# Kernel optimization log

Hardware: AMD Instinct MI355X
Metric: run time of the kernel (lower is better)

## Reference

```python
import jax, jax.numpy as jnp
import numpy as np

EMBED = 1024
HEADS = 16
HEAD_DIM = EMBED // HEADS
WINDOW = 1024
HALF = WINDOW // 2  # effective causal lookback per token is HALF (window positions > i are masked)
SCALE = HEAD_DIM ** -0.5
B, T = 2, 4096


def setup_inputs() -> dict:
    key = jax.random.key(0)
    ks = jax.random.split(key, 11)
    f = jnp.float32
    return {
        'query': jax.random.normal(ks[0], (B, T, EMBED), f),
        'key':   jax.random.normal(ks[1], (B, T, EMBED), f),
        'value': jax.random.normal(ks[2], (B, T, EMBED), f),
        'wq': jax.random.normal(ks[3], (EMBED, EMBED), f) * 0.02,
        'bq': jax.random.normal(ks[4], (EMBED,), f) * 0.02,
        'wk': jax.random.normal(ks[5], (EMBED, EMBED), f) * 0.02,
        'bk': jax.random.normal(ks[6], (EMBED,), f) * 0.02,
        'wv': jax.random.normal(ks[7], (EMBED, EMBED), f) * 0.02,
        'bv': jax.random.normal(ks[8], (EMBED,), f) * 0.02,
        'wo': jax.random.normal(ks[9], (EMBED, EMBED), f) * 0.02,
        'bo': jax.random.normal(ks[10], (EMBED,), f) * 0.02,
    }


def _sliding_window_attn(q, k, v):
    # q,k,v: [B,H,T,D]; each query i attends to keys j with i-HALF <= j <= i.
    # Blocked formulation with block size Bk=HALF: block b attends to blocks b-1 and b.
    Bq, H, Tq, D = q.shape
    Bk = HALF
    nb = Tq // Bk  # T chosen to be a multiple of HALF
    qb = q.reshape(Bq, H, nb, Bk, D)

    def ctx(x):
        xb = x.reshape(Bq, H, nb, Bk, D)
        prev = jnp.concatenate([jnp.zeros_like(xb[:, :, :1]), xb[:, :, :-1]], axis=2)
        return jnp.concatenate([prev, xb], axis=3)  # [B,H,nb,2Bk,D]

    kc, vc = ctx(k), ctx(v)
    scores = jnp.einsum('bhnrd,bhncd->bhnrc', qb, kc)  # [B,H,nb,Bk,2Bk]
    r = jnp.arange(Bk)[:, None]          # query pos within block
    c = jnp.arange(2 * Bk)[None, :]      # key pos within [prev|cur] context
    # global diff = (Bk + r) - c; valid iff 0 <= diff <= HALF  <=>  r <= c <= r + Bk
    band = (c >= r) & (c <= r + Bk)      # [Bk, 2Bk]
    b_idx = jnp.arange(nb)[:, None, None]
    valid = band[None] & ((b_idx > 0) | (c[None] >= Bk))  # first block has no prev keys
    neg_inf = jnp.finfo(jnp.float32).min
    scores = jnp.where(valid[None, None], scores.astype(jnp.float32), neg_inf)
    attn = jax.nn.softmax(scores, axis=-1).astype(q.dtype)
    out = jnp.einsum('bhnrc,bhncd->bhnrd', attn, vc)
    return out.reshape(Bq, H, Tq, D)


def reference(query, key, value, wq, bq, wk, bk, wv, bv, wo, bo):
    Bq, Tq, C = query.shape
    split = lambda x: x.reshape(Bq, Tq, HEADS, HEAD_DIM).transpose(0, 2, 1, 3)
    q = split(jnp.einsum('btc,oc->bto', query, wq) + bq) * SCALE
    k = split(jnp.einsum('btc,oc->bto', key, wk) + bk)
    v = split(jnp.einsum('btc,oc->bto', value, wv) + bv)
    o = _sliding_window_attn(q, k, v)                       # [B,H,T,D]
    o = o.transpose(0, 2, 1, 3).reshape(Bq, Tq, C)
    return jnp.einsum('btc,oc->bto', o, wo) + bo
```

## Files before the change

### kernel.cpp

```cpp
#include <hip/hip_runtime.h>
#include <hip/hip_bf16.h>

typedef __attribute__((ext_vector_type(8))) short short8;
typedef __attribute__((ext_vector_type(4))) float f32x4;

__device__ __forceinline__ unsigned short f2bf(float f) {
  union { float f; unsigned int u; } x; x.f = f;
  unsigned int r = x.u + 0x7fffu + ((x.u >> 16) & 1u);
  return (unsigned short)(r >> 16);
}

__device__ __forceinline__ float fexp2(float x) {
#if __has_builtin(__builtin_amdgcn_exp2f)
  return __builtin_amdgcn_exp2f(x);
#else
  float r;
  asm("v_exp_f32 %0, %1" : "=v"(r) : "v"(x));
  return r;
#endif
}

#define MFMA16(a, b, c) __builtin_amdgcn_mfma_f32_16x16x32_bf16((a), (b), (c), 0, 0, 0)

__device__ __forceinline__ void gload_lds16(const void* g, void* l) {
  __builtin_amdgcn_global_load_lds((const __attribute__((address_space(1))) void*)g,
                                   (__attribute__((address_space(3))) void*)l, 16, 0, 0);
}

#define WAIT_VM(n) asm volatile("s_waitcnt vmcnt(" #n ")" ::: "memory")
#define RAW_BAR() asm volatile("s_barrier" ::: "memory")

__device__ __forceinline__ void p32swap(unsigned int& a, unsigned int& b) {
  asm volatile("v_permlane32_swap_b32 %0, %1" : "+v"(a), "+v"(b));
}
__device__ __forceinline__ void p16swap(unsigned int& a, unsigned int& b) {
  asm volatile("v_permlane16_swap_b32 %0, %1" : "+v"(a), "+v"(b));
}

#define QSCALE 0.1803368801111244f

__global__ __launch_bounds__(256) void cvt_all(
    const float* __restrict__ q, const float* __restrict__ k,
    const float* __restrict__ v, const float* __restrict__ w0,
    const float* __restrict__ w1, const float* __restrict__ w2,
    const float* __restrict__ w3, unsigned short* __restrict__ Tb,
    unsigned short* __restrict__ Kc, unsigned short* __restrict__ Vc,
    unsigned short* __restrict__ Wb) {
  const int lin = blockIdx.x;
  const float* src;
  unsigned short* dst;
  int i0;
  if (lin < 4096)        { src = q;  dst = Tb;                i0 = lin; }
  else if (lin < 8192)   { src = k;  dst = Kc;                i0 = lin - 4096; }
  else if (lin < 12288)  { src = v;  dst = Vc;                i0 = lin - 8192; }
  else if (lin < 12800)  { src = w0; dst = Wb;                i0 = lin - 12288; }
  else if (lin < 13312)  { src = w1; dst = Wb + (1u << 20);   i0 = lin - 12800; }
  else if (lin < 13824)  { src = w2; dst = Wb + (2u << 20);   i0 = lin - 13312; }
  else                   { src = w3; dst = Wb + (3u << 20);   i0 = lin - 13824; }
  const size_t i = (size_t)i0 * 256 + threadIdx.x;
  const float4* p = (const float4*)src + 2 * i;
  float4 a = p[0], b = p[1];
  ushort4 lo, hi;
  lo.x = f2bf(a.x); lo.y = f2bf(a.y); lo.z = f2bf(a.z); lo.w = f2bf(a.w);
  hi.x = f2bf(b.x); hi.y = f2bf(b.y); hi.z = f2bf(b.z); hi.w = f2bf(b.w);
  ((ushort4*)dst)[2 * i] = lo;
  ((ushort4*)dst)[2 * i + 1] = hi;
}

template <bool SWAP>
__device__ __forceinline__ void gemm_core(const unsigned short* __restrict__ A,
                                          const unsigned short* __restrict__ W,
                                          unsigned short (*As)[128 * 64],
                                          unsigned short (*Bs)[128 * 64],
                                          int bm, int bn, f32x4 (&acc)[2][4]) {
  const int tid = threadIdx.x, lane = tid & 63, wid = tid >> 6;
  const int g = lane >> 4, li = lane & 15;
  const int wr = wid >> 1, wc = wid & 1;
  const int trow = tid >> 3;
  const int js = (tid & 7) ^ (trow & 7);

  auto stage = [&](int kt, int pb) {
    const int k0 = kt << 6;
    #pragma unroll
    for (int r = 0; r < 2; ++r) {
      const int row = r * 64 + trow;
      gload_lds16(A + (size_t)(bm * 128 + row) * 1024 + k0 + js * 8,
                  &As[pb][(r * 64 + wid * 8) * 64]);
      gload_lds16(W + (size_t)(bn * 128 + row) * 1024 + k0 + js * 8,
                  &Bs[pb][(r * 64 + wid * 8) * 64]);
    }
  };

  stage(0, 0);
  int p = 0;
  for (int kt = 0; kt < 16; ++kt) {
    if (kt < 15) {
      stage(kt + 1, p ^ 1);
      WAIT_VM(4);
    } else {
      WAIT_VM(0);
    }
    RAW_BAR();
    #pragma unroll
    for (int kst = 0; kst < 2; ++kst) {
      short8 a[2], b[4];
      #pragma unroll
      for (int mi = 0; mi < 2; ++mi) {
        const int row = wr * 32 + mi * 16 + li;
        a[mi] = *(const short8*)((const char*)&As[p][0] + row * 128 +
                                 (((kst * 4 + g) ^ (li & 7)) << 4));
      }
      #pragma unroll
      for (int ni = 0; ni < 4; ++ni) {
        const int row = wc * 64 + ni * 16 + li;
        b[ni] = *(const short8*)((const char*)&Bs[p][0] + row * 128 +
                                 (((kst * 4 + g) ^ (li & 7)) << 4));
      }
      __builtin_amdgcn_s_setprio(1);
      #pragma unroll
      for (int mi = 0; mi < 2; ++mi)
        #pragma unroll
        for (int ni = 0; ni < 4; ++ni) {
          if constexpr (SWAP)
            acc[mi][ni] = MFMA16(b[ni], a[mi], acc[mi][ni]);
          else
            acc[mi][ni] = MFMA16(a[mi], b[ni], acc[mi][ni]);
        }
      __builtin_amdgcn_s_setprio(0);
    }
    RAW_BAR();
    p ^= 1;
  }
}

__global__ __launch_bounds__(512) void qkv_gemm(
    const unsigned short* __restrict__ Aq, const unsigned short* __restrict__ Ak,
    const unsigned short* __restrict__ Av, const unsigned short* __restrict__ Wb,
    const float* __restrict__ bq, const float* __restrict__ bk,
    const float* __restrict__ bv, unsigned short* __restrict__ Qw,
    unsigned short* __restrict__ Kw, unsigned short* __restrict__ Vw) {
  __shared__ unsigned short As[2][128 * 64];
  __shared__ unsigned short Bs[2][128 * 64];
  const int z = blockIdx.z;
  const int bm = blockIdx.x, bn = blockIdx.y;
  const unsigned short* A = (z == 0) ? Aq : (z == 1) ? Ak : Av;
  const unsigned short* W = Wb + ((size_t)z << 20);
  const float* bias = (z == 0) ? bq : (z == 1) ? bk : bv;
  unsigned short* outp = (z == 0) ? Qw : (z == 1) ? Kw : Vw;

  const int tid = threadIdx.x, lane = tid & 63, wid = tid >> 6;
  const int g = lane >> 4, li = lane & 15;
  const int wr = wid >> 1, wc = wid & 1;

  f32x4 acc[2][4] = {};
  if (z == 2)
    gemm_core<true>(A, W, As, Bs, bm, bn, acc);
  else
    gemm_core<false>(A, W, As, Bs, bm, bn, acc);

  if (z == 2) {
    #pragma unroll
    for (int mi = 0; mi < 2; ++mi) {
      const int mm = bm * 128 + wr * 32 + mi * 16 + li;
      const int b_ = mm >> 12, t_ = mm & 4095;
      #pragma unroll
      for (int ni = 0; ni < 4; ++ni)
        #pragma unroll
        for (int r = 0; r < 4; ++r) {
          const int nn = bn * 128 + wc * 64 + ni * 16 + g * 4 + r;
          const int h_ = nn >> 6, d_ = nn & 63;
          float v = acc[mi][ni][r] + bias[nn];
          outp[(((size_t)(b_ * 16 + h_) * 64 + d_) << 12) + t_] = f2bf(v);
        }
    }
  } else {
    const float scale = (z == 0) ? QSCALE : 1.0f;
    #pragma unroll
    for (int mi = 0; mi < 2; ++mi)
      #pragma unroll
      for (int ni = 0; ni < 4; ++ni) {
        const int nn = bn * 128 + wc * 64 + ni * 16 + li;
        const float bv_ = bias[nn];
        #pragma unroll
        for (int r = 0; r < 4; ++r) {
          const int mm = bm * 128 + wr * 32 + mi * 16 + g * 4 + r;
          const float v = (acc[mi][ni][r] + bv_) * scale;
          const int b_ = mm >> 12, t_ = mm & 4095, h_ = nn >> 6, d_ = nn & 63;
          outp[(((size_t)(b_ * 16 + h_) * 4096 + t_) << 6) + d_] = f2bf(v);
        }
      }
  }
}

__global__ __launch_bounds__(512) void out_gemm(const unsigned short* __restrict__ A,
                                                const unsigned short* __restrict__ W,
                                                const float* __restrict__ bias,
                                                float* __restrict__ outp) {
  __shared__ unsigned short As[2][128 * 64];
  __shared__ unsigned short Bs[2][128 * 64];
  const int bm = blockIdx.x, bn = blockIdx.y;
  const int tid = threadIdx.x, lane = tid & 63, wid = tid >> 6;
  const int g = lane >> 4, li = lane & 15;
  const int wr = wid >> 1, wc = wid & 1;
  f32x4 acc[2][4] = {};
  gemm_core<false>(A, W, As, Bs, bm, bn, acc);
  #pragma unroll
  for (int mi = 0; mi < 2; ++mi)
    #pragma unroll
    for (int ni = 0; ni < 4; ++ni) {
      const int nn = bn * 128 + wc * 64 + ni * 16 + li;
      const float bv_ = bias[nn];
      #pragma unroll
      for (int r = 0; r < 4; ++r) {
        const int mm = bm * 128 + wr * 32 + mi * 16 + g * 4 + r;
        outp[(size_t)mm * 1024 + nn] = acc[mi][ni][r] + bv_;
      }
    }
}

__global__ __launch_bounds__(256) void swa_attn(const unsigned short* __restrict__ Q,
                                                const unsigned short* __restrict__ K,
                                                const unsigned short* __restrict__ V,
                                                unsigned short* __restrict__ O) {
  __shared__ unsigned short Kb[2][4096];
  __shared__ unsigned short Vb[2][4096];
  const int tid = threadIdx.x, lane = tid & 63, w = tid >> 6;
  const int g = lane >> 4, li = lane & 15;
  const int lin = blockIdx.x;
  const int xcd = lin & 7;
  const int rest = lin >> 3;
  const int qoff = rest & 7;
  const int grp = rest >> 3;
  const int G = xcd * 16 + grp;
  const int hb = G & 31;
  const int qb = (G >> 5) * 8 + qoff;
  const int qs = qb << 7;
  const int h = hb & 15, b = hb >> 4;
  const int bh = b * 16 + h;
  const unsigned short* Qh = Q + ((size_t)bh << 18);
  const unsigned short* Kh = K + ((size_t)bh << 18);
  const unsigned short* Vh = V + ((size_t)bh << 18);

  short8 qa[2][2];
  #pragma unroll
  for (int qt = 0; qt < 2; ++qt)
    #pragma unroll
    for (int kst = 0; kst < 2; ++kst)
      qa[qt][kst] =
          *(const short8*)&Qh[((size_t)(qs + w * 32 + qt * 16 + li) << 6) + kst * 32 + g * 8];

  const short8 vone = {0x3F80, 0x3F80, 0x3F80, 0x3F80, 0x3F80, 0x3F80, 0x3F80, 0x3F80};
  f32x4 o[2][4] = {};
  f32x4 lac[2] = {};
  const int c0 = (qs >= 512) ? 0 : ((512 - qs) >> 6);

  const int srow_hi = lane >> 3;
  const int sj = lane & 7;

  auto stage = [&](int c, int pb) {
    const int ks = qs - 512 + (c << 6);
    #pragma unroll
    for (int i = 0; i < 2; ++i) {
      const int seg = w + i * 4;
      const int row = seg * 8 + srow_hi;
      const int jsw = sj ^ (row & 7);
      gload_lds16(Kh + (((size_t)(ks + row)) << 6) + jsw * 8, &Kb[pb][seg * 512]);
      gload_lds16(Vh + (((size_t)row) << 12) + ks + jsw * 8, &Vb[pb][seg * 512]);
    }
  };

  int p = 0;
  stage(c0, 0);

  for (int c = c0; c <= 9; ++c) {
    if (c < 9) {
      stage(c + 1, p ^ 1);
      WAIT_VM(4);
    } else {
      WAIT_VM(0);
    }
    RAW_BAR();
    const int cb = c << 6;
    const bool anyq = (cb + 63 >= w * 32) && (cb <= w * 32 + 543);
    if (anyq) {
      short8 kf[4][2], vf[4][2];
      #pragma unroll
      for (int nt = 0; nt < 4; ++nt) {
        const int row = nt * 16 + li, rx = li & 7;
        #pragma unroll
        for (int kst = 0; kst < 2; ++kst) {
          const int byt = row * 128 + (((kst * 4 + g) ^ rx) << 4);
          kf[nt][kst] = *(const short8*)((const char*)&Kb[p][0] + byt);
          vf[nt][kst] = *(const short8*)((const char*)&Vb[p][0] + byt);
        }
      }
      #pragma unroll
      for (int qt = 0; qt < 2; ++qt) {
        const int base = w * 32 + qt * 16;
        if (cb + 63 < base || cb > base + 527) continue;
        f32x4 s[4];
        __builtin_amdgcn_s_setprio(1);
        #pragma unroll
        for (int nt = 0; nt < 4; ++nt) {
          f32x4 z = {};
          s[nt] = MFMA16(kf[nt][0], qa[qt][0], z);
          s[nt] = MFMA16(kf[nt][1], qa[qt][1], s[nt]);
        }
        __builtin_amdgcn_s_setprio(0);
        if (cb < base + 16 || cb + 63 > base + 512) {
          #pragma unroll
          for (int nt = 0; nt < 4; ++nt)
            #pragma unroll
            for (int r = 0; r < 4; ++r) {
              const int t1 = cb + nt * 16 + g * 4 + r - base;
              if (t1 < li || t1 > 512 + li) s[nt][r] = -3e38f;
            }
        }
        unsigned int pw[4][2];
        #pragma unroll
        for (int nt = 0; nt < 4; ++nt) {
          float2 ab; ab.x = fexp2(s[nt][0]); ab.y = fexp2(s[nt][1]);
          float2 cd; cd.x = fexp2(s[nt][2]); cd.y = fexp2(s[nt][3]);
          union { __hip_bfloat162 h2; unsigned int u; } u0, u1;
          u0.h2 = __float22bfloat162_rn(ab);
          u1.h2 = __float22bfloat162_rn(cd);
          pw[nt][0] = u0.u;
          pw[nt][1] = u1.u;
        }
        short8 pbf[2];
        #pragma unroll
        for (int kst = 0; kst < 2; ++kst) {
          unsigned int A0 = pw[2 * kst][0], B0 = pw[2 * kst + 1][0];
          unsigned int A1 = pw[2 * kst][1], B1 = pw[2 * kst + 1][1];
          p32swap(A0, B0);
          p32swap(A1, B1);
          p16swap(A0, B0);
          p16swap(A1, B1);
          union { unsigned int u[4]; short8 s8; } pb_;
          pb_.u[0] = A0;
          pb_.u[1] = A1;
          pb_.u[2] = B0;
          pb_.u[3] = B1;
          pbf[kst] = pb_.s8;
        }
        __builtin_amdgcn_s_setprio(1);
        lac[qt] = MFMA16(vone, pbf[0], lac[qt]);
        lac[qt] = MFMA16(vone, pbf[1], lac[qt]);
        #pragma unroll
        for (int dt = 0; dt < 4; ++dt) {
          o[qt][dt] = MFMA16(vf[dt][0], pbf[0], o[qt][dt]);
          o[qt][dt] = MFMA16(vf[dt][1], pbf[1], o[qt][dt]);
        }
        __builtin_amdgcn_s_setprio(0);
      }
    }
    RAW_BAR();
    p ^= 1;
  }

  #pragma unroll
  for (int qt = 0; qt < 2; ++qt) {
    const float inv = 1.0f / lac[qt][0];
    const int t_ = qs + w * 32 + qt * 16 + li;
    #pragma unroll
    for (int dt = 0; dt < 4; ++dt) {
      ushort4 u;
      u.x = f2bf(o[qt][dt][0] * inv); u.y = f2bf(o[qt][dt][1] * inv);
      u.z = f2bf(o[qt][dt][2] * inv); u.w = f2bf(o[qt][dt][3] * inv);
      *(ushort4*)&O[((size_t)(b * 4096 + t_) << 10) + h * 64 + dt * 16 + g * 4] = u;
    }
  }
}

extern "C" void kernel_launch(void* const* d_in, const int* in_sizes, int n_in,
                              void* d_out, int out_size, void* d_ws, size_t ws_size,
                              hipStream_t stream) {
  const float* q_in = (const float*)d_in[0];
  const float* k_in = (const float*)d_in[1];
  const float* v_in = (const float*)d_in[2];
  const float* wq = (const float*)d_in[3];
  const float* bq = (const float*)d_in[4];
  const float* wk = (const float*)d_in[5];
  const float* bk = (const float*)d_in[6];
  const float* wv = (const float*)d_in[7];
  const float* bv = (const float*)d_in[8];
  const float* wo = (const float*)d_in[9];
  const float* bo = (const float*)d_in[10];

  unsigned short* Qw = (unsigned short*)d_ws;
  unsigned short* Kw = Qw + (size_t)8388608;
  unsigned short* Vw = Kw + (size_t)8388608;
  unsigned short* Tb = Vw + (size_t)8388608;
  unsigned short* Wb = Tb + (size_t)8388608;
  unsigned short* Kc = (unsigned short*)d_out;
  unsigned short* Vc = Kc + (size_t)8388608;

  dim3 bb(256), bg(512);
  cvt_all<<<14336, bb, 0, stream>>>(q_in, k_in, v_in, wq, wk, wv, wo,
                                    Tb, Kc, Vc, Wb);
  qkv_gemm<<<dim3(64, 8, 3), bg, 0, stream>>>(Tb, Kc, Vc, Wb, bq, bk, bv,
                                              Qw, Kw, Vw);
  swa_attn<<<1024, bb, 0, stream>>>(Qw, Kw, Vw, Tb);
  out_gemm<<<dim3(64, 8), bg, 0, stream>>>(Tb, Wb + (3u << 20), bo,
                                           (float*)d_out);
}
```

Before: 152.0 us.

## Double attention query tile to 256 rows per block with 8 waves

The sliding-window attention kernel now runs 512-thread blocks, each covering 256 queries instead of 128. K/V are staged 128 keys at a time (two 64-key sub-chunks per double-buffered stage) into doubled LDS buffers. Each staged K/V window is therefore shared by twice as many queries, which cuts redundant K/V global loads and the number of barrier rounds. In exchange the grid halves to 512 blocks, LDS per block doubles, and waves at the edges of the block sit idle for more of the key chunks.

```diff
diff --git a/kernel.cpp b/kernel.cpp
--- a/kernel.cpp
+++ b/kernel.cpp
@@ -218,12 +218,12 @@
     }
 }
 
-__global__ __launch_bounds__(256) void swa_attn(const unsigned short* __restrict__ Q,
+__global__ __launch_bounds__(512) void swa_attn(const unsigned short* __restrict__ Q,
                                                 const unsigned short* __restrict__ K,
                                                 const unsigned short* __restrict__ V,
                                                 unsigned short* __restrict__ O) {
-  __shared__ unsigned short Kb[2][4096];
-  __shared__ unsigned short Vb[2][4096];
+  __shared__ unsigned short Kb[2][8192];
+  __shared__ unsigned short Vb[2][8192];
   const int tid = threadIdx.x, lane = tid & 63, w = tid >> 6;
   const int g = lane >> 4, li = lane & 15;
   const int lin = blockIdx.x;
@@ -231,10 +231,10 @@
   const int rest = lin >> 3;
   const int qoff = rest & 7;
   const int grp = rest >> 3;
-  const int G = xcd * 16 + grp;
+  const int G = xcd * 8 + grp;
   const int hb = G & 31;
   const int qb = (G >> 5) * 8 + qoff;
-  const int qs = qb << 7;
+  const int qs = qb << 8;
   const int h = hb & 15, b = hb >> 4;
   const int bh = b * 16 + h;
   const unsigned short* Qh = Q + ((size_t)bh << 18);
@@ -253,109 +253,115 @@
   f32x4 o[2][4] = {};
   f32x4 lac[2] = {};
   const int c0 = (qs >= 512) ? 0 : ((512 - qs) >> 6);
+  const int p0 = c0 >> 1;
 
   const int srow_hi = lane >> 3;
   const int sj = lane & 7;
 
-  auto stage = [&](int c, int pb) {
-    const int ks = qs - 512 + (c << 6);
-    #pragma unroll
-    for (int i = 0; i < 2; ++i) {
-      const int seg = w + i * 4;
-      const int row = seg * 8 + srow_hi;
+  auto stage = [&](int pi, int pb) {
+    const int ks0 = qs - 512 + (pi << 7);
+    #pragma unroll
+    for (int s = 0; s < 2; ++s) {
+      const int row = w * 8 + srow_hi;
       const int jsw = sj ^ (row & 7);
-      gload_lds16(Kh + (((size_t)(ks + row)) << 6) + jsw * 8, &Kb[pb][seg * 512]);
-      gload_lds16(Vh + (((size_t)row) << 12) + ks + jsw * 8, &Vb[pb][seg * 512]);
+      gload_lds16(Kh + (((size_t)(ks0 + s * 64 + row)) << 6) + jsw * 8,
+                  &Kb[pb][s * 4096 + w * 512]);
+      gload_lds16(Vh + (((size_t)row) << 12) + ks0 + s * 64 + jsw * 8,
+                  &Vb[pb][s * 4096 + w * 512]);
     }
   };
 
-  int p = 0;
-  stage(c0, 0);
-
-  for (int c = c0; c <= 9; ++c) {
-    if (c < 9) {
-      stage(c + 1, p ^ 1);
+  int pb = 0;
+  stage(p0, 0);
+
+  for (int pi = p0; pi <= 5; ++pi) {
+    if (pi < 5) {
+      stage(pi + 1, pb ^ 1);
       WAIT_VM(4);
     } else {
       WAIT_VM(0);
     }
     RAW_BAR();
-    const int cb = c << 6;
-    const bool anyq = (cb + 63 >= w * 32) && (cb <= w * 32 + 543);
-    if (anyq) {
-      short8 kf[4][2], vf[4][2];
-      #pragma unroll
-      for (int nt = 0; nt < 4; ++nt) {
-        const int row = nt * 16 + li, rx = li & 7;
+    #pragma unroll
+    for (int s = 0; s < 2; ++s) {
+      const int c = 2 * pi + s;
+      const int cb = c << 6;
+      const bool anyq = (cb + 63 >= w * 32) && (cb <= w * 32 + 543);
+      if (anyq) {
+        short8 kf[4][2], vf[4][2];
         #pragma unroll
-        for (int kst = 0; kst < 2; ++kst) {
-          const int byt = row * 128 + (((kst * 4 + g) ^ rx) << 4);
-          kf[nt][kst] = *(const short8*)((const char*)&Kb[p][0] + byt);
-          vf[nt][kst] = *(const short8*)((const char*)&Vb[p][0] + byt);
+        for (int nt = 0; nt < 4; ++nt) {
+          const int row = nt * 16 + li, rx = li & 7;
+          #pragma unroll
+          for (int kst = 0; kst < 2; ++kst) {
+            const int byt = s * 8192 + row * 128 + (((kst * 4 + g) ^ rx) << 4);
+            kf[nt][kst] = *(const short8*)((const char*)&Kb[pb][0] + byt);
+            vf[nt][kst] = *(const short8*)((const char*)&Vb[pb][0] + byt);
+          }
+        }
+        #pragma unroll
+        for (int qt = 0; qt < 2; ++qt) {
+          const int base = w * 32 + qt * 16;
+          if (cb + 63 < base || cb > base + 527) continue;
+          f32x4 sv[4];
+          __builtin_amdgcn_s_setprio(1);
+          #pragma unroll
+          for (int nt = 0; nt < 4; ++nt) {
+            f32x4 z = {};
+            sv[nt] = MFMA16(kf[nt][0], qa[qt][0], z);
+            sv[nt] = MFMA16(kf[nt][1], qa[qt][1], sv[nt]);
+          }
+          __builtin_amdgcn_s_setprio(0);
+          if (cb < base + 16 || cb + 63 > base + 512) {
+            #pragma unroll
+            for (int nt = 0; nt < 4; ++nt)
+              #pragma unroll
+              for (int r = 0; r < 4; ++r) {
+                const int t1 = cb + nt * 16 + g * 4 + r - base;
+                if (t1 < li || t1 > 512 + li) sv[nt][r] = -3e38f;
+              }
+          }
+          unsigned int pw[4][2];
+          #pragma unroll
+          for (int nt = 0; nt < 4; ++nt) {
+            float2 ab; ab.x = fexp2(sv[nt][0]); ab.y = fexp2(sv[nt][1]);
+            float2 cd; cd.x = fexp2(sv[nt][2]); cd.y = fexp2(sv[nt][3]);
+            union { __hip_bfloat162 h2; unsigned int u; } u0, u1;
+            u0.h2 = __float22bfloat162_rn(ab);
+            u1.h2 = __float22bfloat162_rn(cd);
+            pw[nt][0] = u0.u;
+            pw[nt][1] = u1.u;
+          }
+          short8 pbf[2];
+          #pragma unroll
+          for (int kst = 0; kst < 2; ++kst) {
+            unsigned int A0 = pw[2 * kst][0], B0 = pw[2 * kst + 1][0];
+            unsigned int A1 = pw[2 * kst][1], B1 = pw[2 * kst + 1][1];
+            p32swap(A0, B0);
+            p32swap(A1, B1);
+            p16swap(A0, B0);
+            p16swap(A1, B1);
+            union { unsigned int u[4]; short8 s8; } pb_;
+            pb_.u[0] = A0;
+            pb_.u[1] = A1;
+            pb_.u[2] = B0;
+            pb_.u[3] = B1;
+            pbf[kst] = pb_.s8;
+          }
+          __builtin_amdgcn_s_setprio(1);
+          lac[qt] = MFMA16(vone, pbf[0], lac[qt]);
+          lac[qt] = MFMA16(vone, pbf[1], lac[qt]);
+          #pragma unroll
+          for (int dt = 0; dt < 4; ++dt) {
+            o[qt][dt] = MFMA16(vf[dt][0], pbf[0], o[qt][dt]);
+            o[qt][dt] = MFMA16(vf[dt][1], pbf[1], o[qt][dt]);
+          }
+          __builtin_amdgcn_s_setprio(0);
         }
       }
-      #pragma unroll
-      for (int qt = 0; qt < 2; ++qt) {
-        const int base = w * 32 + qt * 16;
-        if (cb + 63 < base || cb > base + 527) continue;
-        f32x4 s[4];
-        __builtin_amdgcn_s_setprio(1);
-        #pragma unroll
-        for (int nt = 0; nt < 4; ++nt) {
-          f32x4 z = {};
-          s[nt] = MFMA16(kf[nt][0], qa[qt][0], z);
-          s[nt] = MFMA16(kf[nt][1], qa[qt][1], s[nt]);
-        }
-        __builtin_amdgcn_s_setprio(0);
-        if (cb < base + 16 || cb + 63 > base + 512) {
-          #pragma unroll
-          for (int nt = 0; nt < 4; ++nt)
-            #pragma unroll
-            for (int r = 0; r < 4; ++r) {
-              const int t1 = cb + nt * 16 + g * 4 + r - base;
-              if (t1 < li || t1 > 512 + li) s[nt][r] = -3e38f;
-            }
-        }
-        unsigned int pw[4][2];
-        #pragma unroll
-        for (int nt = 0; nt < 4; ++nt) {
-          float2 ab; ab.x = fexp2(s[nt][0]); ab.y = fexp2(s[nt][1]);
-          float2 cd; cd.x = fexp2(s[nt][2]); cd.y = fexp2(s[nt][3]);
-          union { __hip_bfloat162 h2; unsigned int u; } u0, u1;
-          u0.h2 = __float22bfloat162_rn(ab);
-          u1.h2 = __float22bfloat162_rn(cd);
-          pw[nt][0] = u0.u;
-          pw[nt][1] = u1.u;
-        }
-        short8 pbf[2];
-        #pragma unroll
-        for (int kst = 0; kst < 2; ++kst) {
-          unsigned int A0 = pw[2 * kst][0], B0 = pw[2 * kst + 1][0];
-          unsigned int A1 = pw[2 * kst][1], B1 = pw[2 * kst + 1][1];
-          p32swap(A0, B0);
-          p32swap(A1, B1);
-          p16swap(A0, B0);
-          p16swap(A1, B1);
-          union { unsigned int u[4]; short8 s8; } pb_;
-          pb_.u[0] = A0;
-          pb_.u[1] = A1;
-          pb_.u[2] = B0;
-          pb_.u[3] = B1;
-          pbf[kst] = pb_.s8;
-        }
-        __builtin_amdgcn_s_setprio(1);
-        lac[qt] = MFMA16(vone, pbf[0], lac[qt]);
-        lac[qt] = MFMA16(vone, pbf[1], lac[qt]);
-        #pragma unroll
-        for (int dt = 0; dt < 4; ++dt) {
-          o[qt][dt] = MFMA16(vf[dt][0], pbf[0], o[qt][dt]);
-          o[qt][dt] = MFMA16(vf[dt][1], pbf[1], o[qt][dt]);
-        }
-        __builtin_amdgcn_s_setprio(0);
-      }
     }
     RAW_BAR();
-    p ^= 1;
+    pb ^= 1;
   }
 
   #pragma unroll
@@ -400,7 +406,7 @@
                                     Tb, Kc, Vc, Wb);
   qkv_gemm<<<dim3(64, 8, 3), bg, 0, stream>>>(Tb, Kc, Vc, Wb, bq, bk, bv,
                                               Qw, Kw, Vw);
-  swa_attn<<<1024, bb, 0, stream>>>(Qw, Kw, Vw, Tb);
+  swa_attn<<<512, bg, 0, stream>>>(Qw, Kw, Vw, Tb);
   out_gemm<<<dim3(64, 8), bg, 0, stream>>>(Tb, Wb + (3u << 20), bo,
                                            (float*)d_out);
 }
```

Measured after the change: 150.0 us. Within noise of the previous version (-1.4%).
